# Kernel optimization log

Measured on AMD Instinct MI355X. Metric: run time of the kernel, lower is better.

## Reference

```python
import jax, jax.numpy as jnp
import numpy as np
import math


def setup_inputs() -> dict:
    key = jax.random.key(0)
    kq, kk, kv = jax.random.split(key, 3)
    B, H, S, D = 2, 16, 2048, 64
    return {
        "query": jax.random.normal(kq, (B, H, S, D), dtype=jnp.float32),
        "key": jax.random.normal(kk, (B, H, S, D), dtype=jnp.float32),
        "value": jax.random.normal(kv, (B, H, S, D), dtype=jnp.float32),
    }


def reference(query, key, value):
    # scores: [B, H, S, S] = Q K^T / sqrt(d_k)  (naive unfused attention, mask=None)
    d_k = query.shape[-1]
    scores = jnp.einsum("bhqd,bhkd->bhqk", query, key) / math.sqrt(d_k)
    p_attention = jax.nn.softmax(scores, axis=-1)
    out = jnp.einsum("bhqk,bhkd->bhqd", p_attention, value)
    return (out, p_attention)
```

## Files before the change

kernel.cpp:

```cpp
#include <hip/hip_runtime.h>

typedef _Float16 half8 __attribute__((ext_vector_type(8)));
typedef _Float16 half4 __attribute__((ext_vector_type(4)));
typedef float floatx4 __attribute__((ext_vector_type(4)));

__device__ __forceinline__ floatx4 mfma16(half8 a, half8 b, floatx4 c) {
  return __builtin_amdgcn_mfma_f32_16x16x32_f16(a, b, c, 0, 0, 0);
}

constexpr int S_ = 2048;
constexpr int D_ = 64;
constexpr float SCALE = 0.125f;
constexpr int LQ = 72;

__global__ __launch_bounds__(256, 3)
void attn_fused(const float* __restrict__ Q, const float* __restrict__ K,
                const float* __restrict__ V, float* __restrict__ O,
                float* __restrict__ P) {
  __shared__ _Float16 Qs[64 * LQ];
  __shared__ _Float16 Ks[64 * LQ];
  __shared__ _Float16 Vs[64 * LQ];
  __shared__ _Float16 Ps[64 * LQ];

  const int tid  = threadIdx.x;
  const int wave = tid >> 6;
  const int lane = tid & 63;
  const int l16  = lane & 15;
  const int quad = lane >> 4;

  const int bh = blockIdx.x >> 5;
  const int qt = blockIdx.x & 31;

  const float* Qg = Q + ((size_t)bh * S_ + qt * 64) * D_;
  const float* Kg = K + (size_t)bh * S_ * D_;
  const float* Vg = V + (size_t)bh * S_ * D_;
  float* Og = O + ((size_t)bh * S_ + qt * 64) * D_;
  float* Pg = P + (size_t)bh * S_ * S_ + (size_t)qt * 64 * S_;

#pragma unroll
  for (int i = 0; i < 4; ++i) {
    int f4 = tid + (i << 8);
    int r = f4 >> 4, c = (f4 & 15) << 2;
    float4 v = *(const float4*)(Qg + r * D_ + c);
    half4 h; h.x = (_Float16)v.x; h.y = (_Float16)v.y; h.z = (_Float16)v.z; h.w = (_Float16)v.w;
    *(half4*)&Qs[r * LQ + c] = h;
  }
  __syncthreads();

  const int arow = wave * 16 + l16;
  const half8 qa0 = *(const half8*)&Qs[arow * LQ + quad * 8];
  const half8 qa1 = *(const half8*)&Qs[arow * LQ + quad * 8 + 32];

  float rs0 = 0.f, rs1 = 0.f, rs2 = 0.f, rs3 = 0.f;
  for (int kt = 0; kt < 32; ++kt) {
    __syncthreads();
    const float* Kt = Kg + (size_t)kt * 64 * D_;
#pragma unroll
    for (int i = 0; i < 4; ++i) {
      int f4 = tid + (i << 8);
      int r = f4 >> 4, c = (f4 & 15) << 2;
      float4 v = *(const float4*)(Kt + r * D_ + c);
      half4 h; h.x = (_Float16)v.x; h.y = (_Float16)v.y; h.z = (_Float16)v.z; h.w = (_Float16)v.w;
      *(half4*)&Ks[r * LQ + c] = h;
    }
    __syncthreads();
#pragma unroll
    for (int cb = 0; cb < 4; ++cb) {
      half8 b0 = *(const half8*)&Ks[(cb * 16 + l16) * LQ + quad * 8];
      half8 b1 = *(const half8*)&Ks[(cb * 16 + l16) * LQ + quad * 8 + 32];
      floatx4 acc = {0.f, 0.f, 0.f, 0.f};
      acc = mfma16(qa0, b0, acc);
      acc = mfma16(qa1, b1, acc);
      rs0 += __expf(acc[0] * SCALE);
      rs1 += __expf(acc[1] * SCALE);
      rs2 += __expf(acc[2] * SCALE);
      rs3 += __expf(acc[3] * SCALE);
    }
  }
  rs0 += __shfl_xor(rs0, 1); rs0 += __shfl_xor(rs0, 2); rs0 += __shfl_xor(rs0, 4); rs0 += __shfl_xor(rs0, 8);
  rs1 += __shfl_xor(rs1, 1); rs1 += __shfl_xor(rs1, 2); rs1 += __shfl_xor(rs1, 4); rs1 += __shfl_xor(rs1, 8);
  rs2 += __shfl_xor(rs2, 1); rs2 += __shfl_xor(rs2, 2); rs2 += __shfl_xor(rs2, 4); rs2 += __shfl_xor(rs2, 8);
  rs3 += __shfl_xor(rs3, 1); rs3 += __shfl_xor(rs3, 2); rs3 += __shfl_xor(rs3, 4); rs3 += __shfl_xor(rs3, 8);
  const float inv0 = 1.f / rs0, inv1 = 1.f / rs1, inv2 = 1.f / rs2, inv3 = 1.f / rs3;

  floatx4 oacc[4];
#pragma unroll
  for (int cb = 0; cb < 4; ++cb) { floatx4 z = {0.f, 0.f, 0.f, 0.f}; oacc[cb] = z; }

  for (int kt = 0; kt < 32; ++kt) {
    __syncthreads();
    const float* Kt = Kg + (size_t)kt * 64 * D_;
    const float* Vt = Vg + (size_t)kt * 64 * D_;
#pragma unroll
    for (int i = 0; i < 4; ++i) {
      int f4 = tid + (i << 8);
      int r = f4 >> 4, c = (f4 & 15) << 2;
      float4 v = *(const float4*)(Kt + r * D_ + c);
      half4 h; h.x = (_Float16)v.x; h.y = (_Float16)v.y; h.z = (_Float16)v.z; h.w = (_Float16)v.w;
      *(half4*)&Ks[r * LQ + c] = h;
      float4 w = *(const float4*)(Vt + r * D_ + c);
      Vs[(c + 0) * LQ + r] = (_Float16)w.x;
      Vs[(c + 1) * LQ + r] = (_Float16)w.y;
      Vs[(c + 2) * LQ + r] = (_Float16)w.z;
      Vs[(c + 3) * LQ + r] = (_Float16)w.w;
    }
    __syncthreads();
#pragma unroll
    for (int cb = 0; cb < 4; ++cb) {
      half8 b0 = *(const half8*)&Ks[(cb * 16 + l16) * LQ + quad * 8];
      half8 b1 = *(const half8*)&Ks[(cb * 16 + l16) * LQ + quad * 8 + 32];
      floatx4 acc = {0.f, 0.f, 0.f, 0.f};
      acc = mfma16(qa0, b0, acc);
      acc = mfma16(qa1, b1, acc);
      float p0 = __expf(acc[0] * SCALE) * inv0;
      float p1 = __expf(acc[1] * SCALE) * inv1;
      float p2 = __expf(acc[2] * SCALE) * inv2;
      float p3 = __expf(acc[3] * SCALE) * inv3;
      int col = cb * 16 + l16;
      Ps[(wave * 16 + quad * 4 + 0) * LQ + col] = (_Float16)p0;
      Ps[(wave * 16 + quad * 4 + 1) * LQ + col] = (_Float16)p1;
      Ps[(wave * 16 + quad * 4 + 2) * LQ + col] = (_Float16)p2;
      Ps[(wave * 16 + quad * 4 + 3) * LQ + col] = (_Float16)p3;
    }
    __syncthreads();
    float* Pt = Pg + kt * 64;
#pragma unroll
    for (int i = 0; i < 4; ++i) {
      int f4 = tid + (i << 8);
      int r = f4 >> 4, c = (f4 & 15) << 2;
      half4 h = *(const half4*)&Ps[r * LQ + c];
      float4 o; o.x = (float)h.x; o.y = (float)h.y; o.z = (float)h.z; o.w = (float)h.w;
      *(float4*)(Pt + (size_t)r * S_ + c) = o;
    }
    half8 pa0 = *(const half8*)&Ps[arow * LQ + quad * 8];
    half8 pa1 = *(const half8*)&Ps[arow * LQ + quad * 8 + 32];
#pragma unroll
    for (int cb = 0; cb < 4; ++cb) {
      half8 vb0 = *(const half8*)&Vs[(cb * 16 + l16) * LQ + quad * 8];
      half8 vb1 = *(const half8*)&Vs[(cb * 16 + l16) * LQ + quad * 8 + 32];
      oacc[cb] = mfma16(pa0, vb0, oacc[cb]);
      oacc[cb] = mfma16(pa1, vb1, oacc[cb]);
    }
  }

#pragma unroll
  for (int cb = 0; cb < 4; ++cb) {
#pragma unroll
    for (int r = 0; r < 4; ++r) {
      Og[(size_t)(wave * 16 + quad * 4 + r) * D_ + cb * 16 + l16] = oacc[cb][r];
    }
  }
}

extern "C" void kernel_launch(void* const* d_in, const int* in_sizes, int n_in,
                              void* d_out, int out_size, void* d_ws, size_t ws_size,
                              hipStream_t stream) {
  const float* q = (const float*)d_in[0];
  const float* k = (const float*)d_in[1];
  const float* v = (const float*)d_in[2];
  float* out = (float*)d_out;
  float* p   = (float*)d_out + (size_t)2 * 16 * 2048 * 64;
  dim3 grid(32 * 32);
  dim3 block(256);
  attn_fused<<<grid, block, 0, stream>>>(q, k, v, out, p);
}
```

Measured before the change: 707.9 us.

## Double-buffer K/V tiles, enlarge query tile to 128, swizzle V smem, nontemporal P stores

Each block now covers 128 query rows with 512 threads, so every K/V tile loaded from global memory serves twice as many queries. K and V tiles are double-buffered: the next tile is fetched into registers during the current tile's MFMA work and written to the alternate smem buffer, with one barrier per iteration instead of two. V is transposed into shared memory with an XOR swizzle and half2 stores to cut bank conflicts, and the P matrix is written with nontemporal stores. The trade-off is a larger shared-memory footprint, more registers per thread and only 512 blocks, which may lower occupancy.

New measurement: 650.6 us. -8.1%, faster.

```diff
diff --git a/kernel.cpp b/kernel.cpp
--- a/kernel.cpp
+++ b/kernel.cpp
@@ -2,6 +2,7 @@
 
 typedef _Float16 half8 __attribute__((ext_vector_type(8)));
 typedef _Float16 half4 __attribute__((ext_vector_type(4)));
+typedef _Float16 half2_ __attribute__((ext_vector_type(2)));
 typedef float floatx4 __attribute__((ext_vector_type(4)));
 
 __device__ __forceinline__ floatx4 mfma16(half8 a, half8 b, floatx4 c) {
@@ -13,14 +14,38 @@
 constexpr float SCALE = 0.125f;
 constexpr int LQ = 72;
 
-__global__ __launch_bounds__(256, 3)
+__device__ __forceinline__ half4 cvt_h4(float4 v) {
+  half4 h;
+  h.x = (_Float16)v.x; h.y = (_Float16)v.y;
+  h.z = (_Float16)v.z; h.w = (_Float16)v.w;
+  return h;
+}
+
+__device__ __forceinline__ void k_store(_Float16* kbuf, int rq, int cq, float4 f0, float4 f1) {
+  *(half4*)&kbuf[rq * LQ + cq]        = cvt_h4(f0);
+  *(half4*)&kbuf[(rq + 32) * LQ + cq] = cvt_h4(f1);
+}
+
+__device__ __forceinline__ void v_store_swz(_Float16* vbuf, int rq, int cq, float4 f0, float4 f1) {
+  const float* a0 = (const float*)&f0;
+  const float* a1 = (const float*)&f1;
+#pragma unroll
+  for (int j = 0; j < 4; ++j) {
+    int d = cq + j;
+    int addr = d * LQ + (((rq >> 2) ^ ((d >> 2) & 7)) << 3) + ((rq & 3) << 1);
+    half2_ h; h.x = (_Float16)a0[j]; h.y = (_Float16)a1[j];
+    *(half2_*)&vbuf[addr] = h;
+  }
+}
+
+__global__ __launch_bounds__(512, 4)
 void attn_fused(const float* __restrict__ Q, const float* __restrict__ K,
                 const float* __restrict__ V, float* __restrict__ O,
                 float* __restrict__ P) {
-  __shared__ _Float16 Qs[64 * LQ];
-  __shared__ _Float16 Ks[64 * LQ];
-  __shared__ _Float16 Vs[64 * LQ];
-  __shared__ _Float16 Ps[64 * LQ];
+  __shared__ _Float16 Qs[128 * LQ];
+  __shared__ _Float16 Ks[2][64 * LQ];
+  __shared__ _Float16 Vs[2][64 * LQ];
+  __shared__ _Float16 Ps[128 * LQ];
 
   const int tid  = threadIdx.x;
   const int wave = tid >> 6;
@@ -28,22 +53,31 @@
   const int l16  = lane & 15;
   const int quad = lane >> 4;
 
-  const int bh = blockIdx.x >> 5;
-  const int qt = blockIdx.x & 31;
-
-  const float* Qg = Q + ((size_t)bh * S_ + qt * 64) * D_;
+  const int bh = blockIdx.x >> 4;
+  const int qt = blockIdx.x & 15;
+
+  const float* Qg = Q + ((size_t)bh * S_ + qt * 128) * D_;
   const float* Kg = K + (size_t)bh * S_ * D_;
   const float* Vg = V + (size_t)bh * S_ * D_;
-  float* Og = O + ((size_t)bh * S_ + qt * 64) * D_;
-  float* Pg = P + (size_t)bh * S_ * S_ + (size_t)qt * 64 * S_;
+  float* Og = O + ((size_t)bh * S_ + qt * 128) * D_;
+  float* Pg = P + (size_t)bh * S_ * S_ + (size_t)qt * 128 * S_;
+
+  const int rq = tid >> 4;
+  const int cq = (tid & 15) << 2;
 
 #pragma unroll
   for (int i = 0; i < 4; ++i) {
-    int f4 = tid + (i << 8);
-    int r = f4 >> 4, c = (f4 & 15) << 2;
-    float4 v = *(const float4*)(Qg + r * D_ + c);
-    half4 h; h.x = (_Float16)v.x; h.y = (_Float16)v.y; h.z = (_Float16)v.z; h.w = (_Float16)v.w;
-    *(half4*)&Qs[r * LQ + c] = h;
+    int r = rq + (i << 5);
+    float4 v = *(const float4*)(Qg + r * D_ + cq);
+    *(half4*)&Qs[r * LQ + cq] = cvt_h4(v);
+  }
+  {
+    float4 k0 = *(const float4*)(Kg + rq * D_ + cq);
+    float4 k1 = *(const float4*)(Kg + (rq + 32) * D_ + cq);
+    k_store(Ks[0], rq, cq, k0, k1);
+    float4 v0 = *(const float4*)(Vg + (2 * rq) * D_ + cq);
+    float4 v1 = *(const float4*)(Vg + (2 * rq + 1) * D_ + cq);
+    v_store_swz(Vs[0], rq, cq, v0, v1);
   }
   __syncthreads();
 
@@ -53,21 +87,18 @@
 
   float rs0 = 0.f, rs1 = 0.f, rs2 = 0.f, rs3 = 0.f;
   for (int kt = 0; kt < 32; ++kt) {
-    __syncthreads();
-    const float* Kt = Kg + (size_t)kt * 64 * D_;
-#pragma unroll
-    for (int i = 0; i < 4; ++i) {
-      int f4 = tid + (i << 8);
-      int r = f4 >> 4, c = (f4 & 15) << 2;
-      float4 v = *(const float4*)(Kt + r * D_ + c);
-      half4 h; h.x = (_Float16)v.x; h.y = (_Float16)v.y; h.z = (_Float16)v.z; h.w = (_Float16)v.w;
-      *(half4*)&Ks[r * LQ + c] = h;
-    }
-    __syncthreads();
+    const int cur = kt & 1;
+    float4 pk0, pk1;
+    const bool pf = (kt < 31);
+    if (pf) {
+      const float* Kt = Kg + (size_t)(kt + 1) * 64 * D_;
+      pk0 = *(const float4*)(Kt + rq * D_ + cq);
+      pk1 = *(const float4*)(Kt + (rq + 32) * D_ + cq);
+    }
 #pragma unroll
     for (int cb = 0; cb < 4; ++cb) {
-      half8 b0 = *(const half8*)&Ks[(cb * 16 + l16) * LQ + quad * 8];
-      half8 b1 = *(const half8*)&Ks[(cb * 16 + l16) * LQ + quad * 8 + 32];
+      half8 b0 = *(const half8*)&Ks[cur][(cb * 16 + l16) * LQ + quad * 8];
+      half8 b1 = *(const half8*)&Ks[cur][(cb * 16 + l16) * LQ + quad * 8 + 32];
       floatx4 acc = {0.f, 0.f, 0.f, 0.f};
       acc = mfma16(qa0, b0, acc);
       acc = mfma16(qa1, b1, acc);
@@ -76,6 +107,8 @@
       rs2 += __expf(acc[2] * SCALE);
       rs3 += __expf(acc[3] * SCALE);
     }
+    if (pf) k_store(Ks[cur ^ 1], rq, cq, pk0, pk1);
+    __syncthreads();
   }
   rs0 += __shfl_xor(rs0, 1); rs0 += __shfl_xor(rs0, 2); rs0 += __shfl_xor(rs0, 4); rs0 += __shfl_xor(rs0, 8);
   rs1 += __shfl_xor(rs1, 1); rs1 += __shfl_xor(rs1, 2); rs1 += __shfl_xor(rs1, 4); rs1 += __shfl_xor(rs1, 8);
@@ -83,32 +116,37 @@
   rs3 += __shfl_xor(rs3, 1); rs3 += __shfl_xor(rs3, 2); rs3 += __shfl_xor(rs3, 4); rs3 += __shfl_xor(rs3, 8);
   const float inv0 = 1.f / rs0, inv1 = 1.f / rs1, inv2 = 1.f / rs2, inv3 = 1.f / rs3;
 
+  {
+    float4 k0 = *(const float4*)(Kg + rq * D_ + cq);
+    float4 k1 = *(const float4*)(Kg + (rq + 32) * D_ + cq);
+    float4 v0 = *(const float4*)(Vg + (2 * rq) * D_ + cq);
+    float4 v1 = *(const float4*)(Vg + (2 * rq + 1) * D_ + cq);
+    __syncthreads();
+    k_store(Ks[0], rq, cq, k0, k1);
+    v_store_swz(Vs[0], rq, cq, v0, v1);
+  }
+  __syncthreads();
+
   floatx4 oacc[4];
 #pragma unroll
   for (int cb = 0; cb < 4; ++cb) { floatx4 z = {0.f, 0.f, 0.f, 0.f}; oacc[cb] = z; }
 
   for (int kt = 0; kt < 32; ++kt) {
-    __syncthreads();
-    const float* Kt = Kg + (size_t)kt * 64 * D_;
-    const float* Vt = Vg + (size_t)kt * 64 * D_;
-#pragma unroll
-    for (int i = 0; i < 4; ++i) {
-      int f4 = tid + (i << 8);
-      int r = f4 >> 4, c = (f4 & 15) << 2;
-      float4 v = *(const float4*)(Kt + r * D_ + c);
-      half4 h; h.x = (_Float16)v.x; h.y = (_Float16)v.y; h.z = (_Float16)v.z; h.w = (_Float16)v.w;
-      *(half4*)&Ks[r * LQ + c] = h;
-      float4 w = *(const float4*)(Vt + r * D_ + c);
-      Vs[(c + 0) * LQ + r] = (_Float16)w.x;
-      Vs[(c + 1) * LQ + r] = (_Float16)w.y;
-      Vs[(c + 2) * LQ + r] = (_Float16)w.z;
-      Vs[(c + 3) * LQ + r] = (_Float16)w.w;
-    }
-    __syncthreads();
+    const int cur = kt & 1;
+    const bool pf = (kt < 31);
+    float4 pk0, pk1, pv0, pv1;
+    if (pf) {
+      const float* Kt = Kg + (size_t)(kt + 1) * 64 * D_;
+      const float* Vt = Vg + (size_t)(kt + 1) * 64 * D_;
+      pk0 = *(const float4*)(Kt + rq * D_ + cq);
+      pk1 = *(const float4*)(Kt + (rq + 32) * D_ + cq);
+      pv0 = *(const float4*)(Vt + (2 * rq) * D_ + cq);
+      pv1 = *(const float4*)(Vt + (2 * rq + 1) * D_ + cq);
+    }
 #pragma unroll
     for (int cb = 0; cb < 4; ++cb) {
-      half8 b0 = *(const half8*)&Ks[(cb * 16 + l16) * LQ + quad * 8];
-      half8 b1 = *(const half8*)&Ks[(cb * 16 + l16) * LQ + quad * 8 + 32];
+      half8 b0 = *(const half8*)&Ks[cur][(cb * 16 + l16) * LQ + quad * 8];
+      half8 b1 = *(const half8*)&Ks[cur][(cb * 16 + l16) * LQ + quad * 8 + 32];
       floatx4 acc = {0.f, 0.f, 0.f, 0.f};
       acc = mfma16(qa0, b0, acc);
       acc = mfma16(qa1, b1, acc);
@@ -123,24 +161,34 @@
       Ps[(wave * 16 + quad * 4 + 3) * LQ + col] = (_Float16)p3;
     }
     __syncthreads();
+
     float* Pt = Pg + kt * 64;
 #pragma unroll
     for (int i = 0; i < 4; ++i) {
-      int f4 = tid + (i << 8);
-      int r = f4 >> 4, c = (f4 & 15) << 2;
-      half4 h = *(const half4*)&Ps[r * LQ + c];
-      float4 o; o.x = (float)h.x; o.y = (float)h.y; o.z = (float)h.z; o.w = (float)h.w;
-      *(float4*)(Pt + (size_t)r * S_ + c) = o;
-    }
+      int r = rq + (i << 5);
+      half4 h = *(const half4*)&Ps[r * LQ + cq];
+      floatx4 o;
+      o[0] = (float)h.x; o[1] = (float)h.y; o[2] = (float)h.z; o[3] = (float)h.w;
+      __builtin_nontemporal_store(o, (floatx4*)(Pt + (size_t)r * S_ + cq));
+    }
+
     half8 pa0 = *(const half8*)&Ps[arow * LQ + quad * 8];
     half8 pa1 = *(const half8*)&Ps[arow * LQ + quad * 8 + 32];
 #pragma unroll
     for (int cb = 0; cb < 4; ++cb) {
-      half8 vb0 = *(const half8*)&Vs[(cb * 16 + l16) * LQ + quad * 8];
-      half8 vb1 = *(const half8*)&Vs[(cb * 16 + l16) * LQ + quad * 8 + 32];
+      const int dd  = cb * 16 + l16;
+      const int hsw = (dd >> 2) & 7;
+      half8 vb0 = *(const half8*)&Vs[cur][dd * LQ + ((quad ^ hsw) << 3)];
+      half8 vb1 = *(const half8*)&Vs[cur][dd * LQ + (((quad + 4) ^ hsw) << 3)];
       oacc[cb] = mfma16(pa0, vb0, oacc[cb]);
       oacc[cb] = mfma16(pa1, vb1, oacc[cb]);
     }
+
+    if (pf) {
+      k_store(Ks[cur ^ 1], rq, cq, pk0, pk1);
+      v_store_swz(Vs[cur ^ 1], rq, cq, pv0, pv1);
+    }
+    __syncthreads();
   }
 
 #pragma unroll
@@ -160,7 +208,7 @@
   const float* v = (const float*)d_in[2];
   float* out = (float*)d_out;
   float* p   = (float*)d_out + (size_t)2 * 16 * 2048 * 64;
-  dim3 grid(32 * 32);
-  dim3 block(256);
+  dim3 grid(32 * 16);
+  dim3 block(512);
   attn_fused<<<grid, block, 0, stream>>>(q, k, v, out, p);
 }
```
